# Kernel tuning notes

Hardware: AMD Instinct MI355X
Metric: run time of the kernel (lower is better)

## Reference

```python
import jax, jax.numpy as jnp
import numpy as np

B, GRID, D, NF, NC = 4096, 8, 64, 256, 10
N = GRID * GRID          # num_nodes = grid_size**2
LN_EPS = 1e-5            # torch LayerNorm default eps


def _grid_mask():
    m = np.zeros((N, N), np.float32)
    for i in range(N):
        r, c = divmod(i, GRID)
        if r > 0: m[i, i - GRID] = 1
        if r < GRID - 1: m[i, i + GRID] = 1
        if c > 0: m[i, i - 1] = 1
        if c < GRID - 1: m[i, i + 1] = 1
    return jnp.asarray(m)

MASK = _grid_mask()  # static 4-neighbor grid adjacency mask [N,N]


def _ln(x, g, b):
    mu = x.mean(-1, keepdims=True)
    v = ((x - mu) ** 2).mean(-1, keepdims=True)  # biased var, like torch LayerNorm
    return (x - mu) / jnp.sqrt(v + LN_EPS) * g + b


def _regulator(x, h_pre, w_norm, p):
    # HomeostaticRegulator.forward (eval mode: baselines fixed at 0.5 / 1.0)
    var = jnp.var(x, axis=1, ddof=1, keepdims=True)            # torch.var default unbiased=True
    natural_stress = jnp.abs(var - 0.5)
    xs = jnp.sort(x, axis=1)
    smoothness = jnp.abs(xs[:, 1:] - xs[:, :-1]).mean(1, keepdims=True)
    adversarial_stress = jnp.abs(smoothness - 1.0)
    excitation = jnp.abs(h_pre).mean(1, keepdims=True)
    fatigue = jnp.broadcast_to(jnp.reshape(w_norm, (1, 1)), (x.shape[0], 1))
    gradient_proxy = jnp.sqrt((h_pre ** 2).mean(1, keepdims=True))
    s = jnp.concatenate([natural_stress, adversarial_stress, excitation, fatigue, gradient_proxy], axis=1)
    h = jnp.tanh(_ln(s @ p[0].T + p[1], p[2], p[3]))
    h = jnp.tanh(_ln(h @ p[4].T + p[5], p[6], p[7]))
    return jax.nn.sigmoid(h @ p[8].T + p[9])  # [B,3] = metabolism, sensitivity, gate


def _cell(x, W_slow, W_fast, ln_g, ln_b, cp):
    # HomeoContinuumCell.forward, eval mode (no Hebbian buffer update)
    h_raw = jax.lax.stop_gradient(x @ W_slow.T)                 # computed under torch.no_grad
    w_norm = jax.lax.stop_gradient(jnp.sqrt((W_slow ** 2).sum()))
    ctl = _regulator(x, h_raw, w_norm, cp)
    beta = 0.5 + ctl[:, 1:2] * 2.0
    gate = ctl[:, 2:3]
    comb = x @ W_slow.T + (x @ W_fast.T) * gate
    act = comb * jax.nn.sigmoid(beta * comb)
    return _ln(act, ln_g, ln_b)


def _forward(x, W_embed, b_embed, adj_weights, W_slow, W_fast, ln_g, ln_b, W_read, b_read, tp, cp):
    e = x @ W_embed.T + b_embed                                 # [B, N*D]
    e3 = e.reshape(B, N, D)
    # HomeoTopology.get_adjacency with homeostasis (all under no_grad in torch)
    ts = jax.lax.stop_gradient(e.reshape(1, -1))                # flatten whole batch state
    wn = jax.lax.stop_gradient(jnp.sqrt((adj_weights ** 2).sum()))
    ctl = jax.lax.stop_gradient(_regulator(ts, ts, wn, tp))
    ap = ctl[:, 0].mean()                                       # plasticity(=1.0) * mean metabolism
    adj = jax.nn.sigmoid(adj_weights * ap) * MASK
    adj = adj / jnp.clip(adj.sum(1, keepdims=True), 1e-6, None)
    m = jnp.einsum('nm,bmd->bnd', adj, e3)                      # grid message passing
    proc = _cell(m.reshape(B * N, D), W_slow, W_fast, ln_g, ln_b, cp)
    return proc.reshape(B, N * D) @ W_read.T + b_read           # logits [B, NC]


def _reg_params(key, scale=0.2):
    ks = jax.random.split(key, 3)
    return (jax.random.normal(ks[0], (16, 5)) * scale, jnp.zeros(16), jnp.ones(16), jnp.zeros(16),
            jax.random.normal(ks[1], (8, 16)) * scale, jnp.zeros(8), jnp.ones(8), jnp.zeros(8),
            jax.random.normal(ks[2], (3, 8)) * scale, jnp.zeros(3))


def setup_inputs() -> dict:
    key = jax.random.key(0)
    ks = jax.random.split(key, 9)
    inp = {
        'x': jax.random.normal(ks[0], (B, NF)),
        'W_embed': jax.random.normal(ks[1], (N * D, NF)) * (1.0 / np.sqrt(NF)),
        'b_embed': jnp.zeros(N * D),
        'adj_weights': jax.random.normal(ks[2], (N, N)) * 0.1,
        'W_slow': jax.random.normal(ks[3], (D, D)) * (1.4 / np.sqrt(D)),
        'W_fast': jax.random.normal(ks[4], (D, D)) * 0.05,
        'ln_g': jnp.ones(D), 'ln_b': jnp.zeros(D),
        'W_read': jax.random.normal(ks[5], (NC, N * D)) * (1.0 / np.sqrt(N * D)),
        'b_read': jnp.zeros(NC),
    }
    names = ['W1', 'b1', 'g1', 'bb1', 'W2', 'b2', 'g2', 'bb2', 'W3', 'b3']
    for pre, k in (('t', ks[6]), ('c', ks[7])):
        for n, v in zip(names, _reg_params(k)):
            inp[pre + '_' + n] = v
    return inp


def reference(x, W_embed, b_embed, adj_weights, W_slow, W_fast, ln_g, ln_b, W_read, b_read,
              t_W1, t_b1, t_g1, t_bb1, t_W2, t_b2, t_g2, t_bb2, t_W3, t_b3,
              c_W1, c_b1, c_g1, c_bb1, c_W2, c_b2, c_g2, c_bb2, c_W3, c_b3):
    tp = (t_W1, t_b1, t_g1, t_bb1, t_W2, t_b2, t_g2, t_bb2, t_W3, t_b3)
    cp = (c_W1, c_b1, c_g1, c_bb1, c_W2, c_b2, c_g2, c_bb2, c_W3, c_b3)
    return _forward(x, W_embed, b_embed, adj_weights, W_slow, W_fast, ln_g, ln_b, W_read, b_read, tp, cp)
```

## Files before the change

kernel.cpp:

```cpp
#include <hip/hip_runtime.h>

typedef unsigned short u16;
typedef unsigned int   u32;
typedef float f32x4 __attribute__((ext_vector_type(4)));
typedef int   i32x4 __attribute__((ext_vector_type(4)));
typedef int   i32x2 __attribute__((ext_vector_type(2)));
typedef short s8v   __attribute__((ext_vector_type(8)));

__device__ inline u16 f2bf(float f) {
  u32 u = __float_as_uint(f);
  return (u16)((u + 0x7FFFu + ((u >> 16) & 1u)) >> 16);
}
__device__ inline float bf2f(u16 h) { return __uint_as_float(((u32)h) << 16); }

__device__ inline u32 fkey(float f) {
  u32 u = __float_as_uint(f);
  return (u & 0x80000000u) ? ~u : (u | 0x80000000u);
}
__device__ inline float unkey(u32 k) {
  u32 u = (k & 0x80000000u) ? (k & 0x7FFFFFFFu) : ~k;
  return __uint_as_float(u);
}
__device__ inline float fast_tanh(float x) {
  float cx = fminf(fmaxf(x, -15.f), 15.f);
  float e = __expf(2.f * cx);
  return __fdividef(e - 1.f, e + 1.f);
}
__device__ inline float sigm(float x) { return __fdividef(1.f, 1.f + __expf(-x)); }

__device__ inline void gload_lds16(const u16* g, u16* l) {
  __builtin_amdgcn_global_load_lds((const __attribute__((address_space(1))) u32*)g,
                                   (__attribute__((address_space(3))) u32*)l, 16, 0, 0);
}

struct MlpP { const float *W1,*b1,*g1,*bb1,*W2,*b2,*g2,*bb2,*W3,*b3; };

__device__ inline void mlp_eval(const MlpP& p, const float* s, float* ctl) {
  float h1[16];
  float mu = 0.f;
  #pragma unroll
  for (int i = 0; i < 16; ++i) {
    float v = p.b1[i];
    #pragma unroll
    for (int k = 0; k < 5; ++k) v = fmaf(p.W1[i*5+k], s[k], v);
    h1[i] = v; mu += v;
  }
  mu *= (1.0f/16.0f);
  float vv = 0.f;
  #pragma unroll
  for (int i = 0; i < 16; ++i) { float d = h1[i]-mu; vv += d*d; }
  vv *= (1.0f/16.0f);
  float inv = 1.0f/sqrtf(vv + 1e-5f);
  #pragma unroll
  for (int i = 0; i < 16; ++i) h1[i] = fast_tanh((h1[i]-mu)*inv*p.g1[i] + p.bb1[i]);
  float h2[8];
  mu = 0.f;
  #pragma unroll
  for (int o = 0; o < 8; ++o) {
    float v = p.b2[o];
    #pragma unroll
    for (int i = 0; i < 16; ++i) v = fmaf(p.W2[o*16+i], h1[i], v);
    h2[o] = v; mu += v;
  }
  mu *= 0.125f;
  vv = 0.f;
  #pragma unroll
  for (int o = 0; o < 8; ++o) { float d = h2[o]-mu; vv += d*d; }
  vv *= 0.125f;
  inv = 1.0f/sqrtf(vv + 1e-5f);
  #pragma unroll
  for (int o = 0; o < 8; ++o) h2[o] = fast_tanh((h2[o]-mu)*inv*p.g2[o] + p.bb2[o]);
  #pragma unroll
  for (int c = 0; c < 3; ++c) {
    float v = p.b3[c];
    #pragma unroll
    for (int o = 0; o < 8; ++o) v = fmaf(p.W3[c*8+o], h2[o], v);
    ctl[c] = sigm(v);
  }
}

__global__ __launch_bounds__(256) void k_pre(const float* __restrict__ x,
                                             const float* __restrict__ We,
                                             const float* __restrict__ Ws,
                                             const float* __restrict__ Wf,
                                             const float* __restrict__ adjw,
                                             u16* __restrict__ Xb, u16* __restrict__ Wb,
                                             u16* __restrict__ WsB, u16* __restrict__ WfB,
                                             float* __restrict__ S) {
  const int bi = blockIdx.x, t = threadIdx.x;
  if (bi < 2048) {
    const float* src = (bi < 1024) ? x : We;
    u16* dst = (bi < 1024) ? Xb : Wb;
    int i = ((bi & 1023) * 256 + t) * 4;
    f32x4 v = *(const f32x4*)(src + i);
    u16 o[4] = { f2bf(v[0]), f2bf(v[1]), f2bf(v[2]), f2bf(v[3]) };
    *(u32*)(dst + i)     = ((u32)o[1] << 16) | o[0];
    *(u32*)(dst + i + 2) = ((u32)o[3] << 16) | o[2];
  } else {
    #pragma unroll
    for (int m = 0; m < 2; ++m) {
      const float* src = m ? Wf : Ws;
      u16* dst = m ? WfB : WsB;
      int base = t * 16;
      u16 o[16];
      #pragma unroll
      for (int r = 0; r < 4; ++r) {
        f32x4 v = *(const f32x4*)(src + base + r*4);
        o[r*4+0]=f2bf(v[0]); o[r*4+1]=f2bf(v[1]); o[r*4+2]=f2bf(v[2]); o[r*4+3]=f2bf(v[3]);
      }
      #pragma unroll
      for (int r = 0; r < 8; ++r)
        *(u32*)(dst + base + r*2) = ((u32)o[r*2+1] << 16) | o[r*2];
    }
    __shared__ float red2[2][256];
    float a = 0.f, w = 0.f;
    for (int i = t; i < 4096; i += 256) {
      float v = adjw[i]; a = fmaf(v, v, a);
      float u = Ws[i];   w = fmaf(u, u, w);
    }
    red2[0][t] = a; red2[1][t] = w;
    __syncthreads();
    for (int sred = 128; sred > 0; sred >>= 1) {
      if (t < sred) { red2[0][t] += red2[0][t+sred]; red2[1][t] += red2[1][t+sred]; }
      __syncthreads();
    }
    if (t == 0) { S[5] = sqrtf(red2[0][0]); S[7] = sqrtf(red2[1][0]); }
    if (t < 3) S[t] = 0.f;
    if (t == 3) ((u32*)S)[3] = 0xFFFFFFFFu;
    if (t == 4) ((u32*)S)[4] = 0u;
  }
}

__global__ __launch_bounds__(256) void k_gemm(const u16* __restrict__ Xb,
                                              const u16* __restrict__ Wb,
                                              const float* __restrict__ bias,
                                              u16* __restrict__ E,
                                              float* __restrict__ S) {
  __shared__ __align__(16) u16 As[128*64];
  __shared__ __align__(16) u16 Bs[128*64];
  const int t = threadIdx.x;
  const int wv = t >> 6, lane = t & 63;
  const int wr = wv >> 1, wc = wv & 1;
  const int bid = blockIdx.x;
  const int sw = (bid & 7) * 128 + (bid >> 3);
  const int i0 = (sw >> 5) * 128, j0 = (sw & 31) * 128;
  const int rr = lane & 15, q = lane >> 4;
  const int lrow = lane >> 3, lcol = (lane & 7) * 8;
  f32x4 acc[4][4] = {};
  for (int k0 = 0; k0 < 256; k0 += 64) {
    #pragma unroll
    for (int r = 0; r < 4; ++r) {
      const int row = (r*4 + wv)*8 + lrow;
      gload_lds16(Xb + (size_t)(i0 + row)*256 + k0 + lcol, &As[(r*4 + wv)*512]);
      gload_lds16(Wb + (size_t)(j0 + row)*256 + k0 + lcol, &Bs[(r*4 + wv)*512]);
    }
    __syncthreads();
    #pragma unroll
    for (int ks = 0; ks < 2; ++ks) {
      s8v a[4], b[4];
      #pragma unroll
      for (int m = 0; m < 4; ++m) a[m] = *(const s8v*)&As[(wr*64 + m*16 + rr)*64 + ks*32 + q*8];
      #pragma unroll
      for (int n = 0; n < 4; ++n) b[n] = *(const s8v*)&Bs[(wc*64 + n*16 + rr)*64 + ks*32 + q*8];
      #pragma unroll
      for (int m = 0; m < 4; ++m)
        #pragma unroll
        for (int n = 0; n < 4; ++n)
          acc[m][n] = __builtin_amdgcn_mfma_f32_16x16x32_bf16(a[m], b[n], acc[m][n], 0, 0, 0);
    }
    __syncthreads();
  }
  float s = 0.f, ss = 0.f, sa = 0.f, mnv = 1e30f, mxv = -1e30f;
  #pragma unroll
  for (int n = 0; n < 4; ++n) {
    const int col = j0 + wc*64 + n*16 + rr;
    const float bv = bias[col];
    #pragma unroll
    for (int m = 0; m < 4; ++m) {
      const int rowb = i0 + wr*64 + m*16 + q*4;
      #pragma unroll
      for (int r = 0; r < 4; ++r) {
        float v = acc[m][n][r] + bv;
        E[(size_t)(rowb + r)*4096 + col] = f2bf(v);
        s += v; ss = fmaf(v, v, ss); sa += fabsf(v);
        mnv = fminf(mnv, v); mxv = fmaxf(mxv, v);
      }
    }
  }
  #pragma unroll
  for (int off = 32; off; off >>= 1) {
    s += __shfl_xor(s, off); ss += __shfl_xor(ss, off); sa += __shfl_xor(sa, off);
    mnv = fminf(mnv, __shfl_xor(mnv, off));
    mxv = fmaxf(mxv, __shfl_xor(mxv, off));
  }
  __shared__ float red5[4][5];
  if (lane == 0) { red5[wv][0]=s; red5[wv][1]=ss; red5[wv][2]=sa; red5[wv][3]=mnv; red5[wv][4]=mxv; }
  __syncthreads();
  if (t == 0) {
    float S0 = red5[0][0]+red5[1][0]+red5[2][0]+red5[3][0];
    float S1 = red5[0][1]+red5[1][1]+red5[2][1]+red5[3][1];
    float S2 = red5[0][2]+red5[1][2]+red5[2][2]+red5[3][2];
    float Mn = fminf(fminf(red5[0][3],red5[1][3]), fminf(red5[2][3],red5[3][3]));
    float Mx = fmaxf(fmaxf(red5[0][4],red5[1][4]), fmaxf(red5[2][4],red5[3][4]));
    atomicAdd(&S[0], S0); atomicAdd(&S[1], S1); atomicAdd(&S[2], S2);
    atomicMin((u32*)S + 3, fkey(Mn));
    atomicMax((u32*)S + 4, fkey(Mx));
  }
}

__global__ __launch_bounds__(256) void k_cell(const u16* __restrict__ E,
    const u16* __restrict__ WsB, const u16* __restrict__ WfB,
    const float* __restrict__ adjw,
    const float* __restrict__ lng, const float* __restrict__ lnb,
    const float* __restrict__ Wread, const float* __restrict__ bread,
    const float* __restrict__ S,
    const float* tW1, const float* tb1, const float* tg1, const float* tbb1,
    const float* tW2, const float* tb2, const float* tg2, const float* tbb2,
    const float* tW3, const float* tb3,
    const float* cW1, const float* cb1, const float* cg1, const float* cbb1,
    const float* cW2, const float* cb2, const float* cg2, const float* cbb2,
    const float* cW3, const float* cb3,
    float* __restrict__ out) {
  __shared__ __align__(16) u16 ebM[64][72];
  __shared__ __align__(16) u16 WsH[64][72];
  __shared__ __align__(16) u16 WfH[64][72];
  __shared__ __align__(16) float adjcL[256];
  __shared__ __align__(16) float prm[308];
  __shared__ __align__(16) float tprm[308];
  __shared__ __align__(16) float lngL[64], lnbL[64];
  __shared__ float wavp[4][10];
  __shared__ float wncL, apS;

  const int t = threadIdx.x;
  const int wv = t >> 6, lane = t & 63;
  const int b = blockIdx.x;
  const u16* Eb = E + (size_t)b * 4096;

  {
    const int row = t >> 2, c16 = (t & 3) * 16;
    *(i32x4*)&ebM[row][c16]     = *(const i32x4*)(Eb  + row*64 + c16);
    *(i32x4*)&ebM[row][c16 + 8] = *(const i32x4*)(Eb  + row*64 + c16 + 8);
    *(i32x4*)&WsH[row][c16]     = *(const i32x4*)(WsB + row*64 + c16);
    *(i32x4*)&WsH[row][c16 + 8] = *(const i32x4*)(WsB + row*64 + c16 + 8);
    *(i32x4*)&WfH[row][c16]     = *(const i32x4*)(WfB + row*64 + c16);
    *(i32x4*)&WfH[row][c16 + 8] = *(const i32x4*)(WfB + row*64 + c16 + 8);
  }
  for (int i = t; i < 80;  i += 256) { prm[i] = cW1[i]; tprm[i] = tW1[i]; }
  if (t < 16) { prm[80+t]=cb1[t]; prm[96+t]=cg1[t]; prm[112+t]=cbb1[t];
                tprm[80+t]=tb1[t]; tprm[96+t]=tg1[t]; tprm[112+t]=tbb1[t]; }
  for (int i = t; i < 128; i += 256) { prm[128+i] = cW2[i]; tprm[128+i] = tW2[i]; }
  if (t < 8)  { prm[256+t]=cb2[t]; prm[264+t]=cg2[t]; prm[272+t]=cbb2[t];
                tprm[256+t]=tb2[t]; tprm[264+t]=tg2[t]; tprm[272+t]=tbb2[t]; }
  if (t < 24) { prm[280+t] = cW3[t]; tprm[280+t] = tW3[t]; }
  if (t < 3)  { prm[304+t] = cb3[t]; tprm[304+t] = tb3[t]; }
  if (t < 64) { lngL[t] = lng[t]; lnbL[t] = lnb[t]; }
  if (t == 0) wncL = S[7];
  __syncthreads();

  if (t == 0) {
    const float n = 16777216.0f, n1 = 16777215.0f;
    float sum = S[0], sumsq = S[1], sumabs = S[2];
    float mean = sum / n;
    float var = (sumsq - sum*mean) / n1;
    float mn = unkey(((const u32*)S)[3]);
    float mx = unkey(((const u32*)S)[4]);
    float sfv[5];
    sfv[0] = fabsf(var - 0.5f);
    sfv[1] = fabsf((mx - mn)/n1 - 1.0f);
    sfv[2] = sumabs / n;
    sfv[3] = S[5];
    sfv[4] = sqrtf(sumsq / n);
    MlpP p{tprm, tprm+80, tprm+96, tprm+112, tprm+128, tprm+256, tprm+264, tprm+272, tprm+280, tprm+304};
    float ctl[3];
    mlp_eval(p, sfv, ctl);
    apS = ctl[0];
  }
  __syncthreads();

  if (t < 64) {
    const int gr = t >> 3, gc = t & 7;
    const float ap = apS;
    const int nb[4] = { gr>0 ? t-8 : -1, gr<7 ? t+8 : -1, gc>0 ? t-1 : -1, gc<7 ? t+1 : -1 };
    float w4[4]; float rs = 0.f;
    #pragma unroll
    for (int qq = 0; qq < 4; ++qq) {
      w4[qq] = (nb[qq] >= 0) ? sigm(adjw[t*64 + nb[qq]] * ap) : 0.0f;
      rs += w4[qq];
    }
    rs = fmaxf(rs, 1e-6f);
    #pragma unroll
    for (int qq = 0; qq < 4; ++qq) adjcL[t*4 + qq] = w4[qq] / rs;
  }
  __syncthreads();

  float macc[16];
  {
    const int d = lane;
    #pragma unroll
    for (int i = 0; i < 16; ++i) {
      const int n = wv*16 + i;
      const int gr = n >> 3, gc = n & 7;
      const int nb0 = gr > 0 ? n - 8 : 0;
      const int nb1 = gr < 7 ? n + 8 : 0;
      const int nb2 = gc > 0 ? n - 1 : 0;
      const int nb3 = gc < 7 ? n + 1 : 0;
      macc[i] = adjcL[n*4+0]*bf2f(ebM[nb0][d]) + adjcL[n*4+1]*bf2f(ebM[nb1][d])
              + adjcL[n*4+2]*bf2f(ebM[nb2][d]) + adjcL[n*4+3]*bf2f(ebM[nb3][d]);
    }
  }
  __syncthreads();
  #pragma unroll
  for (int i = 0; i < 16; ++i) ebM[wv*16 + i][lane] = f2bf(macc[i]);
  __syncthreads();

  const int rr = lane & 15, q = lane >> 4;
  const int n = wv*16 + rr;
  s8v bm0 = *(const s8v*)&ebM[n][q*8];
  s8v bm1 = *(const s8v*)&ebM[n][32 + q*8];
  f32x4 hs[4], hf[4];
  #pragma unroll
  for (int jt = 0; jt < 4; ++jt) {
    const u16* wsr = &WsH[jt*16 + rr][0];
    const u16* wfr = &WfH[jt*16 + rr][0];
    s8v aw0 = *(const s8v*)(wsr + q*8), aw1 = *(const s8v*)(wsr + 32 + q*8);
    s8v af0 = *(const s8v*)(wfr + q*8), af1 = *(const s8v*)(wfr + 32 + q*8);
    f32x4 z = {0.f, 0.f, 0.f, 0.f};
    hs[jt] = __builtin_amdgcn_mfma_f32_16x16x32_bf16(aw0, bm0, z, 0, 0, 0);
    hs[jt] = __builtin_amdgcn_mfma_f32_16x16x32_bf16(aw1, bm1, hs[jt], 0, 0, 0);
    hf[jt] = __builtin_amdgcn_mfma_f32_16x16x32_bf16(af0, bm0, z, 0, 0, 0);
    hf[jt] = __builtin_amdgcn_mfma_f32_16x16x32_bf16(af1, bm1, hf[jt], 0, 0, 0);
  }

  float s1 = 0.f, s2 = 0.f, mnv = 1e30f, mxv = -1e30f;
  #pragma unroll
  for (int j = 0; j < 8; ++j) {
    float v0 = bf2f((u16)bm0[j]), v1 = bf2f((u16)bm1[j]);
    s1 += v0 + v1;
    s2 = fmaf(v0, v0, s2); s2 = fmaf(v1, v1, s2);
    mnv = fminf(mnv, fminf(v0, v1));
    mxv = fmaxf(mxv, fmaxf(v0, v1));
  }
  float sa = 0.f, sq = 0.f;
  #pragma unroll
  for (int jt = 0; jt < 4; ++jt)
    #pragma unroll
    for (int r = 0; r < 4; ++r) { float v = hs[jt][r]; sa += fabsf(v); sq = fmaf(v, v, sq); }
  #pragma unroll
  for (int off = 16; off <= 32; off <<= 1) {
    s1 += __shfl_xor(s1, off); s2 += __shfl_xor(s2, off);
    sa += __shfl_xor(sa, off); sq += __shfl_xor(sq, off);
    mnv = fminf(mnv, __shfl_xor(mnv, off));
    mxv = fmaxf(mxv, __shfl_xor(mxv, off));
  }
  if (q == 0) {
    float var = (s2 - s1*s1*(1.f/64.f)) * (1.f/63.f);
    f32x4 sv = { fabsf(var - 0.5f),
                 fabsf((mxv - mnv)*(1.f/63.f) - 1.f),
                 sa * (1.f/64.f),
                 sqrtf(sq * (1.f/64.f)) };
    *(f32x4*)&ebM[n][64] = sv;
  }
  __syncthreads();

  if (t < 64) {
    f32x4 sv = *(const f32x4*)&ebM[t][64];
    float sfv[5] = { sv[0], sv[1], sv[2], wncL, sv[3] };
    MlpP p{prm, prm+80, prm+96, prm+112, prm+128, prm+256, prm+264, prm+272, prm+280, prm+304};
    float ctl[3];
    mlp_eval(p, sfv, ctl);
    float* pad = (float*)&ebM[t][64];
    pad[0] = 0.5f + 2.f*ctl[1];
    pad[1] = ctl[2];
  }
  __syncthreads();

  const float beta = ((const float*)&ebM[n][64])[0];
  const float gate = ((const float*)&ebM[n][64])[1];
  float acts[4][4];
  float a1 = 0.f, a2 = 0.f;
  #pragma unroll
  for (int jt = 0; jt < 4; ++jt)
    #pragma unroll
    for (int r = 0; r < 4; ++r) {
      float comb = fmaf(hf[jt][r], gate, hs[jt][r]);
      float sv = comb * sigm(beta * comb);
      acts[jt][r] = sv;
      a1 += sv; a2 = fmaf(sv, sv, a2);
    }
  a1 += __shfl_xor(a1, 16); a2 += __shfl_xor(a2, 16);
  a1 += __shfl_xor(a1, 32); a2 += __shfl_xor(a2, 32);
  float mu = a1 * (1.f/64.f);
  float vvv = a2 * (1.f/64.f) - mu*mu;
  float inv = 1.f / sqrtf(vvv + 1e-5f);
  float racc[10];
  #pragma unroll
  for (int c = 0; c < 10; ++c) racc[c] = 0.f;
  #pragma unroll
  for (int jt = 0; jt < 4; ++jt) {
    f32x4 gv = *(const f32x4*)&lngL[jt*16 + q*4];
    f32x4 bv = *(const f32x4*)&lnbL[jt*16 + q*4];
    float pr[4];
    #pragma unroll
    for (int r = 0; r < 4; ++r) pr[r] = (acts[jt][r] - mu)*inv*gv[r] + bv[r];
    const float* wrb = Wread + n*64 + jt*16 + q*4;
    #pragma unroll
    for (int c = 0; c < 10; ++c) {
      f32x4 w = *(const f32x4*)(wrb + c*4096);
      racc[c] += pr[0]*w[0] + pr[1]*w[1] + pr[2]*w[2] + pr[3]*w[3];
    }
  }
  #pragma unroll
  for (int c = 0; c < 10; ++c) {
    float v = racc[c];
    #pragma unroll
    for (int off = 1; off < 64; off <<= 1) v += __shfl_xor(v, off);
    if (lane == 0) wavp[wv][c] = v;
  }
  __syncthreads();
  if (t < 10) out[(size_t)b*10 + t] = bread[t] + wavp[0][t] + wavp[1][t] + wavp[2][t] + wavp[3][t];
}

extern "C" void kernel_launch(void* const* d_in, const int* in_sizes, int n_in,
                              void* d_out, int out_size, void* d_ws, size_t ws_size,
                              hipStream_t stream) {
  (void)in_sizes; (void)n_in; (void)out_size; (void)ws_size;
  const float* x       = (const float*)d_in[0];
  const float* W_embed = (const float*)d_in[1];
  const float* b_embed = (const float*)d_in[2];
  const float* adjw    = (const float*)d_in[3];
  const float* Wslow   = (const float*)d_in[4];
  const float* Wfast   = (const float*)d_in[5];
  const float* lng     = (const float*)d_in[6];
  const float* lnb     = (const float*)d_in[7];
  const float* Wread   = (const float*)d_in[8];
  const float* bread   = (const float*)d_in[9];
  float* out = (float*)d_out;

  char* ws = (char*)d_ws;
  u16*   Ebf  = (u16*)ws;
  u16*   Xbf  = (u16*)(ws + 33554432);
  u16*   Wbf  = (u16*)(ws + 35651584);
  float* S    = (float*)(ws + 37748736);
  u16*   WsBf = (u16*)(ws + 37752832);
  u16*   WfBf = (u16*)(ws + 37761024);

  hipLaunchKernelGGL(k_pre, dim3(2049), dim3(256), 0, stream,
                     x, W_embed, Wslow, Wfast, adjw, Xbf, Wbf, WsBf, WfBf, S);
  hipLaunchKernelGGL(k_gemm, dim3(1024), dim3(256), 0, stream, Xbf, Wbf, b_embed, Ebf, S);
  hipLaunchKernelGGL(k_cell, dim3(4096), dim3(256), 0, stream, Ebf, WsBf, WfBf, adjw,
                     lng, lnb, Wread, bread, S,
                     (const float*)d_in[10], (const float*)d_in[11], (const float*)d_in[12], (const float*)d_in[13],
                     (const float*)d_in[14], (const float*)d_in[15], (const float*)d_in[16], (const float*)d_in[17],
                     (const float*)d_in[18], (const float*)d_in[19],
                     (const float*)d_in[20], (const float*)d_in[21], (const float*)d_in[22], (const float*)d_in[23],
                     (const float*)d_in[24], (const float*)d_in[25], (const float*)d_in[26], (const float*)d_in[27],
                     (const float*)d_in[28], (const float*)d_in[29], out);
}
```

Baseline: 349.4 us.

## Hoist batch-invariant adjacency/thermo MLP into single-block prep kernel; compute cell MLP redundantly per lane

The global-stats thermo regulator MLP and the normalized adjacency weights were recomputed identically by every one of 4096 cell blocks. They now run once in a tiny one-block kernel that writes the results into the workspace, and the cell kernel just loads them. The per-sample regulator MLP is also evaluated redundantly by every thread of a row instead of by 64 threads, which removes two block barriers and the shared-memory round trip. The cost is an extra kernel launch and more per-thread ALU work and registers in the cell kernel.

```diff
diff --git a/kernel.cpp b/kernel.cpp
--- a/kernel.cpp
+++ b/kernel.cpp
@@ -208,55 +208,13 @@
   }
 }
 
-__global__ __launch_bounds__(256) void k_cell(const u16* __restrict__ E,
-    const u16* __restrict__ WsB, const u16* __restrict__ WfB,
-    const float* __restrict__ adjw,
-    const float* __restrict__ lng, const float* __restrict__ lnb,
-    const float* __restrict__ Wread, const float* __restrict__ bread,
-    const float* __restrict__ S,
+__global__ __launch_bounds__(64) void k_prep(const float* __restrict__ adjw,
     const float* tW1, const float* tb1, const float* tg1, const float* tbb1,
     const float* tW2, const float* tb2, const float* tg2, const float* tbb2,
     const float* tW3, const float* tb3,
-    const float* cW1, const float* cb1, const float* cg1, const float* cbb1,
-    const float* cW2, const float* cb2, const float* cg2, const float* cbb2,
-    const float* cW3, const float* cb3,
-    float* __restrict__ out) {
-  __shared__ __align__(16) u16 ebM[64][72];
-  __shared__ __align__(16) u16 WsH[64][72];
-  __shared__ __align__(16) u16 WfH[64][72];
-  __shared__ __align__(16) float adjcL[256];
-  __shared__ __align__(16) float prm[308];
-  __shared__ __align__(16) float tprm[308];
-  __shared__ __align__(16) float lngL[64], lnbL[64];
-  __shared__ float wavp[4][10];
-  __shared__ float wncL, apS;
-
+    float* __restrict__ S) {
+  __shared__ float apS;
   const int t = threadIdx.x;
-  const int wv = t >> 6, lane = t & 63;
-  const int b = blockIdx.x;
-  const u16* Eb = E + (size_t)b * 4096;
-
-  {
-    const int row = t >> 2, c16 = (t & 3) * 16;
-    *(i32x4*)&ebM[row][c16]     = *(const i32x4*)(Eb  + row*64 + c16);
-    *(i32x4*)&ebM[row][c16 + 8] = *(const i32x4*)(Eb  + row*64 + c16 + 8);
-    *(i32x4*)&WsH[row][c16]     = *(const i32x4*)(WsB + row*64 + c16);
-    *(i32x4*)&WsH[row][c16 + 8] = *(const i32x4*)(WsB + row*64 + c16 + 8);
-    *(i32x4*)&WfH[row][c16]     = *(const i32x4*)(WfB + row*64 + c16);
-    *(i32x4*)&WfH[row][c16 + 8] = *(const i32x4*)(WfB + row*64 + c16 + 8);
-  }
-  for (int i = t; i < 80;  i += 256) { prm[i] = cW1[i]; tprm[i] = tW1[i]; }
-  if (t < 16) { prm[80+t]=cb1[t]; prm[96+t]=cg1[t]; prm[112+t]=cbb1[t];
-                tprm[80+t]=tb1[t]; tprm[96+t]=tg1[t]; tprm[112+t]=tbb1[t]; }
-  for (int i = t; i < 128; i += 256) { prm[128+i] = cW2[i]; tprm[128+i] = tW2[i]; }
-  if (t < 8)  { prm[256+t]=cb2[t]; prm[264+t]=cg2[t]; prm[272+t]=cbb2[t];
-                tprm[256+t]=tb2[t]; tprm[264+t]=tg2[t]; tprm[272+t]=tbb2[t]; }
-  if (t < 24) { prm[280+t] = cW3[t]; tprm[280+t] = tW3[t]; }
-  if (t < 3)  { prm[304+t] = cb3[t]; tprm[304+t] = tb3[t]; }
-  if (t < 64) { lngL[t] = lng[t]; lnbL[t] = lnb[t]; }
-  if (t == 0) wncL = S[7];
-  __syncthreads();
-
   if (t == 0) {
     const float n = 16777216.0f, n1 = 16777215.0f;
     float sum = S[0], sumsq = S[1], sumabs = S[2];
@@ -270,14 +228,13 @@
     sfv[2] = sumabs / n;
     sfv[3] = S[5];
     sfv[4] = sqrtf(sumsq / n);
-    MlpP p{tprm, tprm+80, tprm+96, tprm+112, tprm+128, tprm+256, tprm+264, tprm+272, tprm+280, tprm+304};
+    MlpP p{tW1,tb1,tg1,tbb1,tW2,tb2,tg2,tbb2,tW3,tb3};
     float ctl[3];
     mlp_eval(p, sfv, ctl);
     apS = ctl[0];
   }
   __syncthreads();
-
-  if (t < 64) {
+  {
     const int gr = t >> 3, gc = t & 7;
     const float ap = apS;
     const int nb[4] = { gr>0 ? t-8 : -1, gr<7 ? t+8 : -1, gc>0 ? t-1 : -1, gc<7 ? t+1 : -1 };
@@ -289,8 +246,51 @@
     }
     rs = fmaxf(rs, 1e-6f);
     #pragma unroll
-    for (int qq = 0; qq < 4; ++qq) adjcL[t*4 + qq] = w4[qq] / rs;
-  }
+    for (int qq = 0; qq < 4; ++qq) S[8 + t*4 + qq] = w4[qq] / rs;
+  }
+}
+
+__global__ __launch_bounds__(256) void k_cell(const u16* __restrict__ E,
+    const u16* __restrict__ WsB, const u16* __restrict__ WfB,
+    const float* __restrict__ lng, const float* __restrict__ lnb,
+    const float* __restrict__ Wread, const float* __restrict__ bread,
+    const float* __restrict__ S,
+    const float* cW1, const float* cb1, const float* cg1, const float* cbb1,
+    const float* cW2, const float* cb2, const float* cg2, const float* cbb2,
+    const float* cW3, const float* cb3,
+    float* __restrict__ out) {
+  __shared__ __align__(16) u16 ebM[64][72];
+  __shared__ __align__(16) u16 WsH[64][72];
+  __shared__ __align__(16) u16 WfH[64][72];
+  __shared__ __align__(16) float adjcL[256];
+  __shared__ __align__(16) float prm[308];
+  __shared__ __align__(16) float lngL[64], lnbL[64];
+  __shared__ float wavp[4][10];
+  __shared__ float wncL;
+
+  const int t = threadIdx.x;
+  const int wv = t >> 6, lane = t & 63;
+  const int b = blockIdx.x;
+  const u16* Eb = E + (size_t)b * 4096;
+
+  {
+    const int row = t >> 2, c16 = (t & 3) * 16;
+    *(i32x4*)&ebM[row][c16]     = *(const i32x4*)(Eb  + row*64 + c16);
+    *(i32x4*)&ebM[row][c16 + 8] = *(const i32x4*)(Eb  + row*64 + c16 + 8);
+    *(i32x4*)&WsH[row][c16]     = *(const i32x4*)(WsB + row*64 + c16);
+    *(i32x4*)&WsH[row][c16 + 8] = *(const i32x4*)(WsB + row*64 + c16 + 8);
+    *(i32x4*)&WfH[row][c16]     = *(const i32x4*)(WfB + row*64 + c16);
+    *(i32x4*)&WfH[row][c16 + 8] = *(const i32x4*)(WfB + row*64 + c16 + 8);
+  }
+  adjcL[t] = S[8 + t];
+  for (int i = t; i < 80;  i += 256) prm[i] = cW1[i];
+  if (t < 16) { prm[80+t]=cb1[t]; prm[96+t]=cg1[t]; prm[112+t]=cbb1[t]; }
+  for (int i = t; i < 128; i += 256) prm[128+i] = cW2[i];
+  if (t < 8)  { prm[256+t]=cb2[t]; prm[264+t]=cg2[t]; prm[272+t]=cbb2[t]; }
+  if (t < 24) prm[280+t] = cW3[t];
+  if (t < 3)  prm[304+t] = cb3[t];
+  if (t < 64) { lngL[t] = lng[t]; lnbL[t] = lnb[t]; }
+  if (t == 0) wncL = S[7];
   __syncthreads();
 
   float macc[16];
@@ -352,30 +352,18 @@
     mnv = fminf(mnv, __shfl_xor(mnv, off));
     mxv = fmaxf(mxv, __shfl_xor(mxv, off));
   }
-  if (q == 0) {
-    float var = (s2 - s1*s1*(1.f/64.f)) * (1.f/63.f);
-    f32x4 sv = { fabsf(var - 0.5f),
-                 fabsf((mxv - mnv)*(1.f/63.f) - 1.f),
-                 sa * (1.f/64.f),
-                 sqrtf(sq * (1.f/64.f)) };
-    *(f32x4*)&ebM[n][64] = sv;
-  }
-  __syncthreads();
-
-  if (t < 64) {
-    f32x4 sv = *(const f32x4*)&ebM[t][64];
-    float sfv[5] = { sv[0], sv[1], sv[2], wncL, sv[3] };
-    MlpP p{prm, prm+80, prm+96, prm+112, prm+128, prm+256, prm+264, prm+272, prm+280, prm+304};
-    float ctl[3];
-    mlp_eval(p, sfv, ctl);
-    float* pad = (float*)&ebM[t][64];
-    pad[0] = 0.5f + 2.f*ctl[1];
-    pad[1] = ctl[2];
-  }
-  __syncthreads();
-
-  const float beta = ((const float*)&ebM[n][64])[0];
-  const float gate = ((const float*)&ebM[n][64])[1];
+  float var = (s2 - s1*s1*(1.f/64.f)) * (1.f/63.f);
+  float sfv[5];
+  sfv[0] = fabsf(var - 0.5f);
+  sfv[1] = fabsf((mxv - mnv)*(1.f/63.f) - 1.f);
+  sfv[2] = sa * (1.f/64.f);
+  sfv[3] = wncL;
+  sfv[4] = sqrtf(sq * (1.f/64.f));
+  MlpP p{prm, prm+80, prm+96, prm+112, prm+128, prm+256, prm+264, prm+272, prm+280, prm+304};
+  float ctl[3];
+  mlp_eval(p, sfv, ctl);
+  const float beta = 0.5f + 2.f*ctl[1], gate = ctl[2];
+
   float acts[4][4];
   float a1 = 0.f, a2 = 0.f;
   #pragma unroll
@@ -447,11 +435,12 @@
   hipLaunchKernelGGL(k_pre, dim3(2049), dim3(256), 0, stream,
                      x, W_embed, Wslow, Wfast, adjw, Xbf, Wbf, WsBf, WfBf, S);
   hipLaunchKernelGGL(k_gemm, dim3(1024), dim3(256), 0, stream, Xbf, Wbf, b_embed, Ebf, S);
-  hipLaunchKernelGGL(k_cell, dim3(4096), dim3(256), 0, stream, Ebf, WsBf, WfBf, adjw,
-                     lng, lnb, Wread, bread, S,
+  hipLaunchKernelGGL(k_prep, dim3(1), dim3(64), 0, stream, adjw,
                      (const float*)d_in[10], (const float*)d_in[11], (const float*)d_in[12], (const float*)d_in[13],
                      (const float*)d_in[14], (const float*)d_in[15], (const float*)d_in[16], (const float*)d_in[17],
-                     (const float*)d_in[18], (const float*)d_in[19],
+                     (const float*)d_in[18], (const float*)d_in[19], S);
+  hipLaunchKernelGGL(k_cell, dim3(4096), dim3(256), 0, stream, Ebf, WsBf, WfBf,
+                     lng, lnb, Wread, bread, S,
                      (const float*)d_in[20], (const float*)d_in[21], (const float*)d_in[22], (const float*)d_in[23],
                      (const float*)d_in[24], (const float*)d_in[25], (const float*)d_in[26], (const float*)d_in[27],
                      (const float*)d_in[28], (const float*)d_in[29], out);
```

Measured after the change: 332.8 us. 4.8% less time.
